# Optimization experiments

Hardware: AMD Instinct MI355X
Metric: run time of the kernel (lower is better)

Reference implementation:

```python
import jax, jax.numpy as jnp
import numpy as np

CONTEXT = 3  # config['context']
B, H, W = 8, 256, 256
NBR = 2 * CONTEXT  # number of similarity branches


def _conv(x, w, b):
    # x: [N, Cin, H, W], w: [Cout, Cin, kh, kw], SAME padding, stride 1
    y = jax.lax.conv_general_dilated(x, w, (1, 1), 'SAME',
                                     dimension_numbers=('NCHW', 'OIHW', 'NCHW'))
    return y + b[None, :, None, None]


def setup_inputs() -> dict:
    key = jax.random.key(0)
    ks = jax.random.split(key, 5)
    x = jax.random.normal(ks[0], (B, 2 * CONTEXT + 1, H, W), dtype=jnp.float32)
    # kaiming-ish scaled inits
    W1 = jax.random.normal(ks[1], (NBR, 64, 2, 3, 3), dtype=jnp.float32) * (2.0 / (64 * 9)) ** 0.5
    b1 = jnp.zeros((NBR, 64), dtype=jnp.float32)
    W2 = jax.random.normal(ks[2], (NBR, 1, 64, 1, 1), dtype=jnp.float32) * (2.0 / 1) ** 0.5 * 0.1
    b2 = jnp.zeros((NBR, 1), dtype=jnp.float32)
    Wm = jax.random.normal(ks[3], (7, 7, 3, 3), dtype=jnp.float32) * (2.0 / (7 * 9)) ** 0.5
    bm = jnp.zeros((7,), dtype=jnp.float32)
    return {'x': x, 'W1': W1, 'b1': b1, 'W2': W2, 'b2': b2, 'Wm': Wm, 'bm': bm}


def reference(x, W1, b1, W2, b2, Wm, bm):
    # mode == 'context' path just returns x; this implements the main path.
    base = x[:, CONTEXT:CONTEXT + 1]                                  # [B,1,H,W]
    checks = jnp.concatenate([x[:, :CONTEXT], x[:, CONTEXT + 1:]], axis=1)  # [B,6,H,W]
    check_e = checks[:, :, None]                                      # [B,6,1,H,W]
    base_e = jnp.broadcast_to(base[:, None], check_e.shape)           # [B,6,1,H,W]
    # channel order: pre-frames -> (base, check); post-frames -> (check, base)
    ch0 = jnp.concatenate([base_e[:, :CONTEXT], check_e[:, CONTEXT:]], axis=2 - 2 + 2)  # placeholder
    ch0 = jnp.concatenate([base_e[:, :CONTEXT], check_e[:, CONTEXT:]], axis=1)
    ch1 = jnp.concatenate([check_e[:, :CONTEXT], base_e[:, CONTEXT:]], axis=1)
    pairs = jnp.concatenate([ch0, ch1], axis=2)                       # [B,6,2,H,W]
    pairs = jnp.swapaxes(pairs, 0, 1)                                 # [6,B,2,H,W]

    def branch(pair, w1, bb1, w2, bb2):
        h = jax.nn.relu(_conv(pair, w1, bb1))                         # [B,64,H,W]
        return jax.nn.sigmoid(_conv(h, w2, bb2))                      # [B,1,H,W]

    sims = jax.vmap(branch)(pairs, W1, b1, W2, b2)                    # [6,B,1,H,W]
    weighted = sims[:, :, 0] * jnp.swapaxes(checks, 0, 1)             # [6,B,H,W]
    weighted = jnp.swapaxes(weighted, 0, 1)                           # [B,6,H,W]
    combined = jnp.concatenate([weighted[:, :CONTEXT], base, weighted[:, CONTEXT:]], axis=1)  # [B,7,H,W]
    return _conv(combined, Wm, bm)                                    # [B,7,H,W]
```

## Files before the change

### kernel.cpp

```cpp
#include <hip/hip_runtime.h>
#include <math.h>

#define Bn 8
#define Hn 256
#define Wn 256
#define HW (Hn * Wn)
#define ROWS 8

typedef __attribute__((ext_vector_type(8))) short bf16x8;
typedef __attribute__((ext_vector_type(4))) float f32x4;

__device__ __forceinline__ unsigned int pk_bf16(float lo, float hi) {
  return __builtin_amdgcn_perm(__float_as_uint(hi), __float_as_uint(lo),
                               0x07060302u);
}

__global__ __launch_bounds__(256) void sim_kernel(
    const float* __restrict__ x,
    const float* __restrict__ W1,
    const float* __restrict__ b1,
    const float* __restrict__ W2,
    const float* __restrict__ b2,
    float* __restrict__ comb)
{
  __shared__ float rows[2][10][256];
  __shared__ uint4 imbuf[2][3][256];
  __shared__ uint4 wq[4][64];
  __shared__ uint4 zero16;

  int bi = blockIdx.x;
  int n  = bi >> 8;
  int b  = (bi >> 5) & 7;
  int h0 = (bi & 31) * ROWS;
  int cc = (n < 3) ? n : n + 1;
  int t = threadIdx.x;

  const float* xb     = x + (size_t)b * 7 * HW;
  const float* basep  = xb + 3 * HW;
  const float* checkp = xb + (size_t)cc * HW;

  {
    int f = t >> 6, qq = (t >> 4) & 3, m = t & 15;
    int ch = 16 * f + m;
    int bsrc = (n < 3) ? 0 : 1;
    const float* wch = W1 + ((size_t)(n * 64 + ch)) * 18;
    unsigned int kv[4];
#pragma unroll
    for (int jj = 0; jj < 4; ++jj) {
      int k0 = qq * 8 + jj * 2, k1 = k0 + 1;
      float v0 = 0.f, v1 = 0.f;
      if (k0 < 18) {
        int src = (k0 < 9) ? bsrc : 1 - bsrc;
        v0 = wch[src * 9 + (k0 < 9 ? k0 : k0 - 9)];
      }
      if (k1 < 18) {
        int src = (k1 < 9) ? bsrc : 1 - bsrc;
        v1 = wch[src * 9 + (k1 < 9 ? k1 : k1 - 9)];
      }
      kv[jj] = pk_bf16(v0, v1);
    }
    wq[f][(qq << 4) + m] = make_uint4(kv[0], kv[1], kv[2], kv[3]);
  }
  if (t == 0) zero16 = make_uint4(0u, 0u, 0u, 0u);

  int lane = t & 63, wvid = t >> 6;
  int q = lane >> 4, m_ = lane & 15;
  float w2v[4][4], b1v[4][4];
#pragma unroll
  for (int f = 0; f < 4; ++f) {
    float4 tw = *(const float4*)&W2[n * 64 + 16 * f + 4 * q];
    float4 tb = *(const float4*)&b1[n * 64 + 16 * f + 4 * q];
    w2v[f][0] = tw.x; w2v[f][1] = tw.y; w2v[f][2] = tw.z; w2v[f][3] = tw.w;
    b1v[f][0] = tb.x; b1v[f][1] = tb.y; b1v[f][2] = tb.z; b1v[f][3] = tb.w;
  }
  float bb = b2[n];

  {
    int col = (t & 63) << 2;
#pragma unroll
    for (int it = 0; it < 5; ++it) {
      int rowflat = it * 4 + (t >> 6);
      int pl = (rowflat >= 10) ? 1 : 0;
      int j  = rowflat - pl * 10;
      int hh = h0 - 1 + j;
      const float* src = pl ? checkp : basep;
      float4 val = make_float4(0.f, 0.f, 0.f, 0.f);
      if ((unsigned)hh < (unsigned)Hn) val = *(const float4*)(src + hh * Wn + col);
      *(float4*)&rows[pl][j][col] = val;
    }
  }
  __syncthreads();

  bf16x8 afrag[4];
#pragma unroll
  for (int f = 0; f < 4; ++f) afrag[f] = *(const bf16x8*)&wq[f][lane];

  float* combcc = comb + ((size_t)b * 7 + cc) * HW;
  float* comb3  = comb + ((size_t)b * 7 + 3) * HW;

  auto pack = [&](int hh, int dst) {
    int lr = hh - h0 + 1;
    float v[18];
#pragma unroll
    for (int pl = 0; pl < 2; ++pl) {
#pragma unroll
      for (int rr = 0; rr < 3; ++rr) {
        const float* rp = rows[pl][lr - 1 + rr];
        v[pl * 9 + rr * 3 + 0] = (t > 0) ? rp[t - 1] : 0.f;
        v[pl * 9 + rr * 3 + 1] = rp[t];
        v[pl * 9 + rr * 3 + 2] = (t < 255) ? rp[t + 1] : 0.f;
      }
    }
    if (n == 0) comb3[hh * Wn + t] = v[4];
    unsigned int kv[9];
#pragma unroll
    for (int j = 0; j < 9; ++j) kv[j] = pk_bf16(v[2 * j], v[2 * j + 1]);
    imbuf[dst][0][t] = make_uint4(kv[0], kv[1], kv[2], kv[3]);
    imbuf[dst][1][t] = make_uint4(kv[4], kv[5], kv[6], kv[7]);
    imbuf[dst][2][t] = make_uint4(kv[8], 0u, 0u, 0u);
  };

  pack(h0, 0);
  __syncthreads();

#pragma unroll 2
  for (int r = 0; r < ROWS; ++r) {
    int h = h0 + r;
    int cbuf = r & 1;
    if (r < ROWS - 1) pack(h + 1, 1 - cbuf);

    float g[4];
#pragma unroll
    for (int i = 0; i < 4; ++i) {
      int px = (wvid * 4 + i) * 16 + m_;

      f32x4 acc[4];
#pragma unroll
      for (int f = 0; f < 4; ++f) {
        acc[f][0] = b1v[f][0]; acc[f][1] = b1v[f][1];
        acc[f][2] = b1v[f][2]; acc[f][3] = b1v[f][3];
      }

      const uint4* baddr = (q < 3) ? &imbuf[cbuf][q][px] : &zero16;
      bf16x8 bfrag = *(const bf16x8*)baddr;
#pragma unroll
      for (int f = 0; f < 4; ++f)
        acc[f] = __builtin_amdgcn_mfma_f32_16x16x32_bf16(afrag[f], bfrag,
                                                         acc[f], 0, 0, 0);

      float sp = 0.f;
#pragma unroll
      for (int f = 0; f < 4; ++f)
#pragma unroll
        for (int rr = 0; rr < 4; ++rr)
          sp = fmaf(w2v[f][rr], fmaxf(acc[f][rr], 0.f), sp);
      sp += __shfl_xor(sp, 16, 64);
      sp += __shfl_xor(sp, 32, 64);
      sp += bb;

      float e = __builtin_amdgcn_exp2f(sp * -1.442695041f);
      g[i] = __builtin_amdgcn_rcpf(1.f + e);
    }

    int hi = lane >> 4;
    float gsel = (hi == 0) ? g[0] : (hi == 1) ? g[1] : (hi == 2) ? g[2] : g[3];
    int pxs = wvid * 64 + lane;
    int lr = r + 1;
    combcc[h * Wn + pxs] = gsel * rows[1][lr][pxs];
    __syncthreads();
  }
}

__global__ __launch_bounds__(256) void mix_kernel(
    const float* __restrict__ comb,
    const float* __restrict__ Wm,
    const float* __restrict__ bm,
    float* __restrict__ out)
{
  int idx = blockIdx.x * 256 + threadIdx.x;
  int w0 = (idx & 127) << 1;
  int h  = (idx >> 7) & (Hn - 1);
  int b  = idx >> 15;
  const float* cbase = comb + (size_t)b * 7 * HW;

  float acc[7][2];
#pragma unroll
  for (int oc = 0; oc < 7; ++oc) {
    float bv = bm[oc];
    acc[oc][0] = bv;
    acc[oc][1] = bv;
  }

#pragma unroll 1
  for (int ic = 0; ic < 7; ++ic) {
    float win[3][4];
    const float* plane = cbase + (size_t)ic * HW;
#pragma unroll
    for (int r = 0; r < 3; ++r) {
      int hh = h - 1 + r;
      bool okh = (unsigned)hh < (unsigned)Hn;
      const float* row = plane + hh * Wn;
      if (okh) {
        float2 mid = *(const float2*)(row + w0);
        win[r][0] = (w0 > 0) ? row[w0 - 1] : 0.f;
        win[r][1] = mid.x;
        win[r][2] = mid.y;
        win[r][3] = (w0 + 2 < Wn) ? row[w0 + 2] : 0.f;
      } else {
        win[r][0] = win[r][1] = win[r][2] = win[r][3] = 0.f;
      }
    }
#pragma unroll
    for (int oc = 0; oc < 7; ++oc) {
      const float* wp = Wm + (oc * 7 + ic) * 9;
#pragma unroll
      for (int dy = 0; dy < 3; ++dy) {
#pragma unroll
        for (int dx = 0; dx < 3; ++dx) {
          float wvv = wp[dy * 3 + dx];
          acc[oc][0] = fmaf(wvv, win[dy][0 + dx], acc[oc][0]);
          acc[oc][1] = fmaf(wvv, win[dy][1 + dx], acc[oc][1]);
        }
      }
    }
  }

  float* ob = out + (size_t)b * 7 * HW + h * Wn + w0;
#pragma unroll
  for (int oc = 0; oc < 7; ++oc)
    *(float2*)(ob + (size_t)oc * HW) = make_float2(acc[oc][0], acc[oc][1]);
}

extern "C" void kernel_launch(void* const* d_in, const int* in_sizes, int n_in,
                              void* d_out, int out_size, void* d_ws, size_t ws_size,
                              hipStream_t stream) {
  const float* x  = (const float*)d_in[0];
  const float* W1 = (const float*)d_in[1];
  const float* b1 = (const float*)d_in[2];
  const float* W2 = (const float*)d_in[3];
  const float* b2 = (const float*)d_in[4];
  const float* Wm = (const float*)d_in[5];
  const float* bm = (const float*)d_in[6];
  float* out  = (float*)d_out;
  float* comb = (float*)d_ws;

  sim_kernel<<<6 * 8 * (Hn / ROWS), 256, 0, stream>>>(x, W1, b1, W2, b2, comb);
  mix_kernel<<<1024, 256, 0, stream>>>(comb, Wm, bm, out);
}
```

Measured before the change: 131.0 us.

## Gather bf16 im2col fragments directly from padded LDS rows; tile mix conv in LDS

The sim kernel no longer builds a double-buffered im2col buffer each row with per-row barriers. Each lane now reads its fragment words straight from padded shared-memory rows through precomputed offsets and packs them to bf16 in registers, which removes the per-row __syncthreads. The mix kernel now stages a 4-row tile of all 7 input planes, with halo and padding, in shared memory. Each thread computes 4 outputs per row with vectorized loads and stores instead of scattered global reads. The cost is more LDS reads per MFMA fragment in the sim kernel and a large shared-memory footprint in the mix kernel, which may limit occupancy.

```diff
diff --git a/kernel.cpp b/kernel.cpp
--- a/kernel.cpp
+++ b/kernel.cpp
@@ -6,13 +6,17 @@
 #define Wn 256
 #define HW (Hn * Wn)
 #define ROWS 8
+#define RP 264
 
 typedef __attribute__((ext_vector_type(8))) short bf16x8;
 typedef __attribute__((ext_vector_type(4))) float f32x4;
 
+__device__ __forceinline__ unsigned int pk_bits(unsigned int lo,
+                                                unsigned int hi) {
+  return __builtin_amdgcn_perm(hi, lo, 0x07060302u);
+}
 __device__ __forceinline__ unsigned int pk_bf16(float lo, float hi) {
-  return __builtin_amdgcn_perm(__float_as_uint(hi), __float_as_uint(lo),
-                               0x07060302u);
+  return pk_bits(__float_as_uint(lo), __float_as_uint(hi));
 }
 
 __global__ __launch_bounds__(256) void sim_kernel(
@@ -23,10 +27,8 @@
     const float* __restrict__ b2,
     float* __restrict__ comb)
 {
-  __shared__ float rows[2][10][256];
-  __shared__ uint4 imbuf[2][3][256];
+  __shared__ float rowsF[2 * 10 * RP];
   __shared__ uint4 wq[4][64];
-  __shared__ uint4 zero16;
 
   int bi = blockIdx.x;
   int n  = bi >> 8;
@@ -61,7 +63,6 @@
     }
     wq[f][(qq << 4) + m] = make_uint4(kv[0], kv[1], kv[2], kv[3]);
   }
-  if (t == 0) zero16 = make_uint4(0u, 0u, 0u, 0u);
 
   int lane = t & 63, wvid = t >> 6;
   int q = lane >> 4, m_ = lane & 15;
@@ -79,16 +80,40 @@
     int col = (t & 63) << 2;
 #pragma unroll
     for (int it = 0; it < 5; ++it) {
-      int rowflat = it * 4 + (t >> 6);
-      int pl = (rowflat >= 10) ? 1 : 0;
-      int j  = rowflat - pl * 10;
+      int rf = it * 4 + (t >> 6);
+      int pl = (rf >= 10) ? 1 : 0;
+      int j  = rf - pl * 10;
       int hh = h0 - 1 + j;
       const float* src = pl ? checkp : basep;
       float4 val = make_float4(0.f, 0.f, 0.f, 0.f);
-      if ((unsigned)hh < (unsigned)Hn) val = *(const float4*)(src + hh * Wn + col);
-      *(float4*)&rows[pl][j][col] = val;
-    }
-  }
+      if ((unsigned)hh < (unsigned)Hn)
+        val = *(const float4*)(src + hh * Wn + col);
+      *(float4*)&rowsF[rf * RP + 4 + col] = val;
+    }
+    if (t < 20) {
+      rowsF[t * RP + 3] = 0.f;
+      rowsF[t * RP + 260] = 0.f;
+    }
+    if (t == 20) rowsF[0] = 0.f;
+  }
+
+  const unsigned int* rowsU = (const unsigned int*)rowsF;
+  unsigned int addr[8], vbit[8];
+#pragma unroll
+  for (int jh = 0; jh < 8; ++jh) {
+    int k = 8 * q + jh;
+    if (k < 18) {
+      int pl = (k >= 9) ? 1 : 0;
+      int rem = k - 9 * pl;
+      int rr = rem / 3, dx = rem - rr * 3;
+      addr[jh] = (pl * 10 + rr) * RP + 3 + dx + wvid * 64 + m_;
+      vbit[jh] = 1u;
+    } else {
+      addr[jh] = 0u;
+      vbit[jh] = 0u;
+    }
+  }
+
   __syncthreads();
 
   bf16x8 afrag[4];
@@ -97,42 +122,27 @@
 
   float* combcc = comb + ((size_t)b * 7 + cc) * HW;
   float* comb3  = comb + ((size_t)b * 7 + 3) * HW;
-
-  auto pack = [&](int hh, int dst) {
-    int lr = hh - h0 + 1;
-    float v[18];
-#pragma unroll
-    for (int pl = 0; pl < 2; ++pl) {
-#pragma unroll
-      for (int rr = 0; rr < 3; ++rr) {
-        const float* rp = rows[pl][lr - 1 + rr];
-        v[pl * 9 + rr * 3 + 0] = (t > 0) ? rp[t - 1] : 0.f;
-        v[pl * 9 + rr * 3 + 1] = rp[t];
-        v[pl * 9 + rr * 3 + 2] = (t < 255) ? rp[t + 1] : 0.f;
-      }
-    }
-    if (n == 0) comb3[hh * Wn + t] = v[4];
-    unsigned int kv[9];
-#pragma unroll
-    for (int j = 0; j < 9; ++j) kv[j] = pk_bf16(v[2 * j], v[2 * j + 1]);
-    imbuf[dst][0][t] = make_uint4(kv[0], kv[1], kv[2], kv[3]);
-    imbuf[dst][1][t] = make_uint4(kv[4], kv[5], kv[6], kv[7]);
-    imbuf[dst][2][t] = make_uint4(kv[8], 0u, 0u, 0u);
-  };
-
-  pack(h0, 0);
-  __syncthreads();
-
-#pragma unroll 2
+  int pxs = wvid * 64 + lane;
+
+#pragma unroll 1
   for (int r = 0; r < ROWS; ++r) {
     int h = h0 + r;
-    int cbuf = r & 1;
-    if (r < ROWS - 1) pack(h + 1, 1 - cbuf);
 
     float g[4];
 #pragma unroll
     for (int i = 0; i < 4; ++i) {
-      int px = (wvid * 4 + i) * 16 + m_;
+      unsigned int offs = (unsigned)(r * RP + i * 16);
+
+      unsigned int d[8];
+#pragma unroll
+      for (int jh = 0; jh < 8; ++jh)
+        d[jh] = rowsU[addr[jh] + vbit[jh] * offs];
+
+      union { unsigned int u[4]; bf16x8 v; } bu;
+#pragma unroll
+      for (int jj = 0; jj < 4; ++jj)
+        bu.u[jj] = pk_bits(d[2 * jj], d[2 * jj + 1]);
+      bf16x8 bfrag = bu.v;
 
       f32x4 acc[4];
 #pragma unroll
@@ -140,9 +150,6 @@
         acc[f][0] = b1v[f][0]; acc[f][1] = b1v[f][1];
         acc[f][2] = b1v[f][2]; acc[f][3] = b1v[f][3];
       }
-
-      const uint4* baddr = (q < 3) ? &imbuf[cbuf][q][px] : &zero16;
-      bf16x8 bfrag = *(const bf16x8*)baddr;
 #pragma unroll
       for (int f = 0; f < 4; ++f)
         acc[f] = __builtin_amdgcn_mfma_f32_16x16x32_bf16(afrag[f], bfrag,
@@ -164,10 +171,9 @@
 
     int hi = lane >> 4;
     float gsel = (hi == 0) ? g[0] : (hi == 1) ? g[1] : (hi == 2) ? g[2] : g[3];
-    int pxs = wvid * 64 + lane;
-    int lr = r + 1;
-    combcc[h * Wn + pxs] = gsel * rows[1][lr][pxs];
-    __syncthreads();
+    float ccv = rowsF[(10 + r + 1) * RP + 4 + pxs];
+    combcc[h * Wn + pxs] = gsel * ccv;
+    if (n == 0) comb3[h * Wn + pxs] = rowsF[(r + 1) * RP + 4 + pxs];
   }
 }
 
@@ -177,58 +183,72 @@
     const float* __restrict__ bm,
     float* __restrict__ out)
 {
-  int idx = blockIdx.x * 256 + threadIdx.x;
-  int w0 = (idx & 127) << 1;
-  int h  = (idx >> 7) & (Hn - 1);
-  int b  = idx >> 15;
-  const float* cbase = comb + (size_t)b * 7 * HW;
-
-  float acc[7][2];
+  __shared__ float mr[7 * 6 * RP];
+
+  int bi = blockIdx.x;
+  int b  = bi >> 6;
+  int h0 = (bi & 63) << 2;
+  int t = threadIdx.x;
+
+  for (int u = t; u < 42 * 64; u += 256) {
+    int rf = u >> 6;
+    int col = (u & 63) << 2;
+    int ic = rf / 6, j = rf - ic * 6;
+    int hh = h0 - 1 + j;
+    float4 v = make_float4(0.f, 0.f, 0.f, 0.f);
+    if ((unsigned)hh < (unsigned)Hn)
+      v = *(const float4*)(comb + ((size_t)b * 7 + ic) * HW + hh * Wn + col);
+    *(float4*)&mr[rf * RP + 4 + col] = v;
+  }
+  if (t < 42) {
+    mr[t * RP + 3] = 0.f;
+    mr[t * RP + 260] = 0.f;
+  }
+  __syncthreads();
+
+  int r   = t >> 6;
+  int px0 = (t & 63) << 2;
+  int h   = h0 + r;
+
+  float acc[7][4];
 #pragma unroll
   for (int oc = 0; oc < 7; ++oc) {
     float bv = bm[oc];
-    acc[oc][0] = bv;
-    acc[oc][1] = bv;
+#pragma unroll
+    for (int p = 0; p < 4; ++p) acc[oc][p] = bv;
   }
 
 #pragma unroll 1
   for (int ic = 0; ic < 7; ++ic) {
-    float win[3][4];
-    const float* plane = cbase + (size_t)ic * HW;
-#pragma unroll
-    for (int r = 0; r < 3; ++r) {
-      int hh = h - 1 + r;
-      bool okh = (unsigned)hh < (unsigned)Hn;
-      const float* row = plane + hh * Wn;
-      if (okh) {
-        float2 mid = *(const float2*)(row + w0);
-        win[r][0] = (w0 > 0) ? row[w0 - 1] : 0.f;
-        win[r][1] = mid.x;
-        win[r][2] = mid.y;
-        win[r][3] = (w0 + 2 < Wn) ? row[w0 + 2] : 0.f;
-      } else {
-        win[r][0] = win[r][1] = win[r][2] = win[r][3] = 0.f;
-      }
-    }
+    float w[3][12];
+#pragma unroll
+    for (int dy = 0; dy < 3; ++dy) {
+      const float* rp = &mr[(ic * 6 + r + dy) * RP];
+      *(float4*)&w[dy][0] = *(const float4*)(rp + px0);
+      *(float4*)&w[dy][4] = *(const float4*)(rp + px0 + 4);
+      *(float4*)&w[dy][8] = *(const float4*)(rp + px0 + 8);
+    }
+    const float* wp = Wm + ic * 9;
 #pragma unroll
     for (int oc = 0; oc < 7; ++oc) {
-      const float* wp = Wm + (oc * 7 + ic) * 9;
-#pragma unroll
-      for (int dy = 0; dy < 3; ++dy) {
+      const float* wo = wp + oc * 63;
+#pragma unroll
+      for (int dy = 0; dy < 3; ++dy)
 #pragma unroll
         for (int dx = 0; dx < 3; ++dx) {
-          float wvv = wp[dy * 3 + dx];
-          acc[oc][0] = fmaf(wvv, win[dy][0 + dx], acc[oc][0]);
-          acc[oc][1] = fmaf(wvv, win[dy][1 + dx], acc[oc][1]);
+          float wvv = wo[dy * 3 + dx];
+#pragma unroll
+          for (int p = 0; p < 4; ++p)
+            acc[oc][p] = fmaf(wvv, w[dy][3 + p + dx], acc[oc][p]);
         }
-      }
-    }
-  }
-
-  float* ob = out + (size_t)b * 7 * HW + h * Wn + w0;
+    }
+  }
+
+  float* ob = out + (size_t)b * 7 * HW + h * Wn + px0;
 #pragma unroll
   for (int oc = 0; oc < 7; ++oc)
-    *(float2*)(ob + (size_t)oc * HW) = make_float2(acc[oc][0], acc[oc][1]);
+    *(float4*)(ob + (size_t)oc * HW) =
+        make_float4(acc[oc][0], acc[oc][1], acc[oc][2], acc[oc][3]);
 }
 
 extern "C" void kernel_launch(void* const* d_in, const int* in_sizes, int n_in,
@@ -245,5 +265,5 @@
   float* comb = (float*)d_ws;
 
   sim_kernel<<<6 * 8 * (Hn / ROWS), 256, 0, stream>>>(x, W1, b1, W2, b2, comb);
-  mix_kernel<<<1024, 256, 0, stream>>>(comb, Wm, bm, out);
-}
+  mix_kernel<<<8 * (Hn / 4), 256, 0, stream>>>(comb, Wm, bm, out);
+}
```

Result: faster. 121.6 us (-7.2%).
